# Kernel tuning notes

Hardware: AMD Instinct MI355X
Metric: run time of the kernel (lower is better)

Reference implementation:

```python
import jax, jax.numpy as jnp
import numpy as np


def setup_inputs() -> dict:
    key = jax.random.key(0)
    k1, k2, k3, k4, k5 = jax.random.split(key, 5)
    B, D, T = 32, 256, 32       # batch, word_feature_dim, seq_len
    Dh, H, Wd = 128, 128, 128   # image_feature_dim, height, width
    word_features = jax.random.normal(k1, (B, D, T), dtype=jnp.float32)
    image_features = jax.random.normal(k2, (B, Dh, H, Wd), dtype=jnp.float32)
    words_mask = jax.random.randint(k3, (B, T), 0, 2, dtype=jnp.int32)
    W = jax.random.normal(k4, (Dh, D), dtype=jnp.float32) * (1.0 / np.sqrt(D))
    b = jax.random.normal(k5, (Dh,), dtype=jnp.float32) * 0.01
    return {"word_features": word_features, "image_features": image_features,
            "words_mask": words_mask, "W": W, "b": b}


def reference(word_features, image_features, words_mask, W, b):
    B, D, T = word_features.shape
    Dh = image_features.shape[1]
    N = image_features.shape[2] * image_features.shape[3]  # H*W
    # values = fc(word_features^T)^T : [B, Dh, T]
    values = jnp.einsum('bdt,kd->bkt', word_features, W) + b[None, :, None]
    # queries: [B, N, Dh] (flatten spatial)
    queries = image_features.reshape(B, Dh, N)
    # scores S: [B, N, T]
    S = jnp.einsum('bkn,bkt->bnt', queries, values)
    mask = (words_mask != 0)[:, None, :]  # [B,1,T], True => masked
    S = jnp.where(mask, -jnp.inf, S)
    # softmax over seq dim (original: exp / sum(exp)); stable form is same math
    attn_coefficients = jax.nn.softmax(S, axis=2)  # [B, N, T]
    # context vectors: [B, Dh, N]
    attn = jnp.einsum('bkt,bnt->bkn', values, attn_coefficients)
    return attn, attn_coefficients
```

## Files before the change

### kernel.cpp

```cpp
#include <hip/hip_runtime.h>
#include <math.h>

constexpr int Bc  = 32;
constexpr int Dc  = 256;
constexpr int Tc  = 32;
constexpr int DHc = 128;
constexpr int Nc  = 16384;

typedef _Float16 v8hf __attribute__((ext_vector_type(8)));
typedef _Float16 v2hf __attribute__((ext_vector_type(2)));
typedef float    v4f  __attribute__((ext_vector_type(4)));

__global__ __launch_bounds__(256) void values_kernel(
    const float* __restrict__ wf, const float* __restrict__ Wm,
    const float* __restrict__ bias,
    _Float16* __restrict__ vth, _Float16* __restrict__ vtl,
    _Float16* __restrict__ vph)
{
    __shared__ float wfs[Dc * Tc];
    __shared__ float Ws[16 * 260];

    const int tid = threadIdx.x;
    const int b   = blockIdx.x >> 3;
    const int k0  = (blockIdx.x & 7) * 16;

    {
        const float4* src = (const float4*)(wf + (size_t)b * Dc * Tc);
        float4* dst = (float4*)wfs;
        #pragma unroll
        for (int i = 0; i < 8; ++i) dst[tid + 256 * i] = src[tid + 256 * i];
    }
    {
        #pragma unroll
        for (int i = 0; i < 4; ++i) {
            int f = tid + 256 * i;
            int row = f >> 6, d4 = f & 63;
            *(float4*)&Ws[row * 260 + 4 * d4] =
                *(const float4*)&Wm[(size_t)(k0 + row) * Dc + 4 * d4];
        }
    }
    __syncthreads();

    const int kl  = tid >> 4;
    const int tt0 = (tid & 15) * 2;
    const int k   = k0 + kl;

    float acc0 = bias[k], acc1 = acc0;
    #pragma unroll
    for (int d4 = 0; d4 < 64; ++d4) {
        const float4 w4 = *(const float4*)&Ws[kl * 260 + 4 * d4];
        #pragma unroll
        for (int j = 0; j < 4; ++j) {
            const float2 f2 = *(const float2*)&wfs[(4 * d4 + j) * Tc + tt0];
            const float wv = (j == 0) ? w4.x : (j == 1) ? w4.y : (j == 2) ? w4.z : w4.w;
            acc0 = fmaf(wv, f2.x, acc0);
            acc1 = fmaf(wv, f2.y, acc1);
        }
    }

    _Float16 vh0 = (_Float16)acc0, vh1 = (_Float16)acc1;
    _Float16 vl0 = (_Float16)(acc0 - (float)vh0);
    _Float16 vl1 = (_Float16)(acc1 - (float)vh1);

    __syncthreads();
    _Float16* sh_h = (_Float16*)wfs;
    _Float16* th_h = sh_h + 16 * 32;
    _Float16* th_l = th_h + 32 * 24;

    sh_h[kl * 32 + tt0]     = vh0;
    sh_h[kl * 32 + tt0 + 1] = vh1;
    th_h[tt0 * 24 + kl]       = vh0;
    th_h[(tt0 + 1) * 24 + kl] = vh1;
    th_l[tt0 * 24 + kl]       = vl0;
    th_l[(tt0 + 1) * 24 + kl] = vl1;
    __syncthreads();

    if (tid < 64) {
        int row = tid >> 2, ch = (tid & 3) * 8;
        *(uint4*)&vph[((size_t)b * DHc + k0 + row) * Tc + ch] =
            *(uint4*)&sh_h[row * 32 + ch];
    } else if (tid < 128) {
        int i = tid - 64; int t = i >> 1, hf = (i & 1) * 8;
        *(uint4*)&vth[((size_t)b * Tc + t) * DHc + k0 + hf] =
            *(uint4*)&th_h[t * 24 + hf];
    } else if (tid < 192) {
        int i = tid - 128; int t = i >> 1, hf = (i & 1) * 8;
        *(uint4*)&vtl[((size_t)b * Tc + t) * DHc + k0 + hf] =
            *(uint4*)&th_l[t * 24 + hf];
    }
}

__device__ __forceinline__ _Float16 pick_half(int u, int sel) {
    unsigned short s = (unsigned short)(sel ? (u >> 16) : u);
    return __builtin_bit_cast(_Float16, s);
}

__global__ __launch_bounds__(256) void attn_kernel(
    const float* __restrict__ img,
    const _Float16* __restrict__ vth, const _Float16* __restrict__ vtl,
    const _Float16* __restrict__ vph,
    const int* __restrict__ mask, float* __restrict__ attn,
    float* __restrict__ coeff)
{
    constexpr int VT_LD = 136;
    constexpr int VP_LD = 40;
    __shared__ __align__(16) _Float16 VTh[Tc * VT_LD];
    __shared__ __align__(16) _Float16 VTl[Tc * VT_LD];
    __shared__ __align__(16) _Float16 VPh[DHc * VP_LD];
    __shared__ float mneg[Tc];

    const int tid   = threadIdx.x;
    const int b     = blockIdx.x >> 6;
    const int strip = blockIdx.x & 63;

    {
        const uint4* sth = (const uint4*)(vth + (size_t)b * Tc * DHc);
        const uint4* stl = (const uint4*)(vtl + (size_t)b * Tc * DHc);
        const uint4* sph = (const uint4*)(vph + (size_t)b * DHc * Tc);
        #pragma unroll
        for (int i = 0; i < 2; ++i) {
            int cid = tid + 256 * i;
            int t = cid >> 4, cc = cid & 15;
            *(uint4*)&VTh[t * VT_LD + 8 * cc] = sth[cid];
            *(uint4*)&VTl[t * VT_LD + 8 * cc] = stl[cid];
            int kk = cid >> 2, c4 = cid & 3;
            *(uint4*)&VPh[kk * VP_LD + 8 * c4] = sph[cid];
        }
        if (tid < Tc) mneg[tid] = mask[b * Tc + tid] ? -INFINITY : 0.0f;
    }
    __syncthreads();

    const int lane = tid & 63;
    const int wave = tid >> 6;
    const int c    = lane & 15;
    const int g    = lane >> 4;

    float madd[2][4];
    #pragma unroll
    for (int tt = 0; tt < 2; ++tt)
        #pragma unroll
        for (int r = 0; r < 4; ++r)
            madd[tt][r] = mneg[16 * tt + 4 * g + r];

    const float* qbase = img  + ((size_t)b * DHc + 8 * g) * Nc + c;
    float*       abase = attn + ((size_t)b * DHc + c) * Nc + 4 * g;
    float*       cbase = coeff + (size_t)b * Nc * Tc;

    const int ls_lo = c + 32 * (g & 1);
    const int sel   = g >> 1;

    #pragma unroll 2
    for (int it = 0; it < 4; ++it) {
        const int n0 = strip * 256 + (it * 4 + wave) * 16;

        const float* qp = qbase + n0;
        v8hf Qh[4], Ql[4];
        #pragma unroll
        for (int ks = 0; ks < 4; ++ks)
            #pragma unroll
            for (int j = 0; j < 8; ++j) {
                float qv = qp[(size_t)(ks * 32 + j) * Nc];
                _Float16 h = (_Float16)qv;
                Qh[ks][j] = h;
                Ql[ks][j] = (_Float16)(qv - (float)h);
            }

        v4f Sh[2], Sl[2];
        #pragma unroll
        for (int tt = 0; tt < 2; ++tt) {
            Sh[tt] = (v4f){0.f, 0.f, 0.f, 0.f};
            Sl[tt] = (v4f){0.f, 0.f, 0.f, 0.f};
        }
        #pragma unroll
        for (int tt = 0; tt < 2; ++tt) {
            const int rowbase = (16 * tt + c) * VT_LD + 8 * g;
            #pragma unroll
            for (int ks = 0; ks < 4; ++ks) {
                v8hf va = *(const v8hf*)&VTh[rowbase + ks * 32];
                v8hf vl = *(const v8hf*)&VTl[rowbase + ks * 32];
                Sh[tt] = __builtin_amdgcn_mfma_f32_16x16x32_f16(va, Qh[ks], Sh[tt], 0, 0, 0);
                Sl[tt] = __builtin_amdgcn_mfma_f32_16x16x32_f16(va, Ql[ks], Sl[tt], 0, 0, 0);
                Sl[tt] = __builtin_amdgcn_mfma_f32_16x16x32_f16(vl, Qh[ks], Sl[tt], 0, 0, 0);
            }
        }

        float p0[4], p1[4];
        float m = -INFINITY;
        #pragma unroll
        for (int r = 0; r < 4; ++r) {
            p0[r] = Sh[0][r] + Sl[0][r] + madd[0][r];
            p1[r] = Sh[1][r] + Sl[1][r] + madd[1][r];
            m = fmaxf(m, fmaxf(p0[r], p1[r]));
        }
        m = fmaxf(m, __shfl_xor(m, 16));
        m = fmaxf(m, __shfl_xor(m, 32));
        float sum = 0.0f;
        #pragma unroll
        for (int r = 0; r < 4; ++r) {
            p0[r] = __expf(p0[r] - m); sum += p0[r];
            p1[r] = __expf(p1[r] - m); sum += p1[r];
        }
        sum += __shfl_xor(sum, 16);
        sum += __shfl_xor(sum, 32);
        const float inv = 1.0f / sum;
        #pragma unroll
        for (int r = 0; r < 4; ++r) { p0[r] *= inv; p1[r] *= inv; }

        float* cp = cbase + (size_t)(n0 + c) * Tc + 4 * g;
        *(float4*)cp        = make_float4(p0[0], p0[1], p0[2], p0[3]);
        *(float4*)(cp + 16) = make_float4(p1[0], p1[1], p1[2], p1[3]);

        v8hf Pb;
        #pragma unroll
        for (int r = 0; r < 4; ++r) {
            v2hf h2; h2[0] = (_Float16)p0[r]; h2[1] = (_Float16)p1[r];
            int u   = __builtin_bit_cast(int, h2);
            int ulo = __shfl(u, ls_lo);
            int uhi = __shfl(u, ls_lo + 16);
            Pb[r]     = pick_half(ulo, sel);
            Pb[4 + r] = pick_half(uhi, sel);
        }

        #pragma unroll
        for (int mt = 0; mt < 8; ++mt) {
            v8hf vb2 = *(const v8hf*)&VPh[(16 * mt + c) * VP_LD + 8 * g];
            v4f o = (v4f){0.f, 0.f, 0.f, 0.f};
            o = __builtin_amdgcn_mfma_f32_16x16x32_f16(Pb, vb2, o, 0, 0, 0);
            float* ap = abase + (size_t)(16 * mt) * Nc + n0;
            *(float4*)ap = make_float4(o[0], o[1], o[2], o[3]);
        }
    }
}

extern "C" void kernel_launch(void* const* d_in, const int* in_sizes, int n_in,
                              void* d_out, int out_size, void* d_ws, size_t ws_size,
                              hipStream_t stream)
{
    const float* wf   = (const float*)d_in[0];
    const float* img  = (const float*)d_in[1];
    const int*   msk  = (const int*)d_in[2];
    const float* Wm   = (const float*)d_in[3];
    const float* bias = (const float*)d_in[4];

    float* attn  = (float*)d_out;
    float* coeff = attn + (size_t)Bc * DHc * Nc;

    _Float16* vth = (_Float16*)d_ws;
    _Float16* vtl = vth + (size_t)Bc * DHc * Tc;
    _Float16* vph = vtl + (size_t)Bc * DHc * Tc;

    values_kernel<<<256, 256, 0, stream>>>(wf, Wm, bias, vth, vtl, vph);
    attn_kernel<<<Bc * 64, 256, 0, stream>>>(img, vth, vtl, vph, msk, attn, coeff);
}
```

Baseline: 534.6 us.

## Switch attention kernel to 32x32x16 MFMA tiles with 32-position waves

Reworks the attention kernel so each wave handles 32 spatial positions using 32x32x16 f16 MFMA instructions instead of 16x16x32, for both the score and the context matmuls. The P-matrix relayout now needs one xor-32 shuffle per pair instead of two indexed shuffles with a half-select, and the softmax reductions drop one cross-lane step. All Q loads are hoisted into a register array before conversion. The aim is fewer MFMA issues and shuffles per position and wider 128-byte row segments per global load, at the cost of higher register pressure from the 16-wide accumulators and the 64-float Q buffer.

New measurement: 524.1 us. Within noise of the previous version (-2.0%).

```diff
diff --git a/kernel.cpp b/kernel.cpp
--- a/kernel.cpp
+++ b/kernel.cpp
@@ -10,6 +10,7 @@
 typedef _Float16 v8hf __attribute__((ext_vector_type(8)));
 typedef _Float16 v2hf __attribute__((ext_vector_type(2)));
 typedef float    v4f  __attribute__((ext_vector_type(4)));
+typedef float    v16f __attribute__((ext_vector_type(16)));
 
 __global__ __launch_bounds__(256) void values_kernel(
     const float* __restrict__ wf, const float* __restrict__ Wm,
@@ -88,11 +89,6 @@
         *(uint4*)&vtl[((size_t)b * Tc + t) * DHc + k0 + hf] =
             *(uint4*)&th_l[t * 24 + hf];
     }
-}
-
-__device__ __forceinline__ _Float16 pick_half(int u, int sel) {
-    unsigned short s = (unsigned short)(sel ? (u >> 16) : u);
-    return __builtin_bit_cast(_Float16, s);
 }
 
 __global__ __launch_bounds__(256) void attn_kernel(
@@ -132,102 +128,108 @@
 
     const int lane = tid & 63;
     const int wave = tid >> 6;
-    const int c    = lane & 15;
-    const int g    = lane >> 4;
-
-    float madd[2][4];
+    const int l31  = lane & 31;
+    const int h    = lane >> 5;
+
+    float madd[16];
     #pragma unroll
-    for (int tt = 0; tt < 2; ++tt)
-        #pragma unroll
-        for (int r = 0; r < 4; ++r)
-            madd[tt][r] = mneg[16 * tt + 4 * g + r];
-
-    const float* qbase = img  + ((size_t)b * DHc + 8 * g) * Nc + c;
-    float*       abase = attn + ((size_t)b * DHc + c) * Nc + 4 * g;
+    for (int r = 0; r < 16; ++r)
+        madd[r] = mneg[(r & 3) + 8 * (r >> 2) + 4 * h];
+
+    const float* qbase = img  + ((size_t)b * DHc + 8 * h) * Nc + l31;
     float*       cbase = coeff + (size_t)b * Nc * Tc;
 
-    const int ls_lo = c + 32 * (g & 1);
-    const int sel   = g >> 1;
-
-    #pragma unroll 2
-    for (int it = 0; it < 4; ++it) {
-        const int n0 = strip * 256 + (it * 4 + wave) * 16;
+    for (int it = 0; it < 2; ++it) {
+        const int n0 = strip * 256 + it * 128 + wave * 32;
 
         const float* qp = qbase + n0;
-        v8hf Qh[4], Ql[4];
-        #pragma unroll
-        for (int ks = 0; ks < 4; ++ks)
+        float q[8][8];
+        #pragma unroll
+        for (int ks = 0; ks < 8; ++ks)
+            #pragma unroll
+            for (int j = 0; j < 8; ++j)
+                q[ks][j] = qp[(size_t)(ks * 16 + j) * Nc];
+
+        v8hf Qh[8], Ql[8];
+        #pragma unroll
+        for (int ks = 0; ks < 8; ++ks)
             #pragma unroll
             for (int j = 0; j < 8; ++j) {
-                float qv = qp[(size_t)(ks * 32 + j) * Nc];
-                _Float16 h = (_Float16)qv;
-                Qh[ks][j] = h;
-                Ql[ks][j] = (_Float16)(qv - (float)h);
+                _Float16 hh = (_Float16)q[ks][j];
+                Qh[ks][j] = hh;
+                Ql[ks][j] = (_Float16)(q[ks][j] - (float)hh);
             }
 
-        v4f Sh[2], Sl[2];
-        #pragma unroll
-        for (int tt = 0; tt < 2; ++tt) {
-            Sh[tt] = (v4f){0.f, 0.f, 0.f, 0.f};
-            Sl[tt] = (v4f){0.f, 0.f, 0.f, 0.f};
-        }
-        #pragma unroll
-        for (int tt = 0; tt < 2; ++tt) {
-            const int rowbase = (16 * tt + c) * VT_LD + 8 * g;
-            #pragma unroll
-            for (int ks = 0; ks < 4; ++ks) {
-                v8hf va = *(const v8hf*)&VTh[rowbase + ks * 32];
-                v8hf vl = *(const v8hf*)&VTl[rowbase + ks * 32];
-                Sh[tt] = __builtin_amdgcn_mfma_f32_16x16x32_f16(va, Qh[ks], Sh[tt], 0, 0, 0);
-                Sl[tt] = __builtin_amdgcn_mfma_f32_16x16x32_f16(va, Ql[ks], Sl[tt], 0, 0, 0);
-                Sl[tt] = __builtin_amdgcn_mfma_f32_16x16x32_f16(vl, Qh[ks], Sl[tt], 0, 0, 0);
-            }
-        }
-
-        float p0[4], p1[4];
+        v16f Sh = {0.f}, Sl = {0.f};
+        #pragma unroll
+        for (int r = 0; r < 16; ++r) { Sh[r] = 0.f; Sl[r] = 0.f; }
+        #pragma unroll
+        for (int ks = 0; ks < 8; ++ks) {
+            v8hf va = *(const v8hf*)&VTh[l31 * VT_LD + ks * 16 + 8 * h];
+            v8hf vl = *(const v8hf*)&VTl[l31 * VT_LD + ks * 16 + 8 * h];
+            Sh = __builtin_amdgcn_mfma_f32_32x32x16_f16(va, Qh[ks], Sh, 0, 0, 0);
+            Sl = __builtin_amdgcn_mfma_f32_32x32x16_f16(va, Ql[ks], Sl, 0, 0, 0);
+            Sl = __builtin_amdgcn_mfma_f32_32x32x16_f16(vl, Qh[ks], Sl, 0, 0, 0);
+        }
+
+        float p[16];
         float m = -INFINITY;
         #pragma unroll
-        for (int r = 0; r < 4; ++r) {
-            p0[r] = Sh[0][r] + Sl[0][r] + madd[0][r];
-            p1[r] = Sh[1][r] + Sl[1][r] + madd[1][r];
-            m = fmaxf(m, fmaxf(p0[r], p1[r]));
-        }
-        m = fmaxf(m, __shfl_xor(m, 16));
+        for (int r = 0; r < 16; ++r) {
+            p[r] = Sh[r] + Sl[r] + madd[r];
+            m = fmaxf(m, p[r]);
+        }
         m = fmaxf(m, __shfl_xor(m, 32));
         float sum = 0.0f;
         #pragma unroll
-        for (int r = 0; r < 4; ++r) {
-            p0[r] = __expf(p0[r] - m); sum += p0[r];
-            p1[r] = __expf(p1[r] - m); sum += p1[r];
-        }
-        sum += __shfl_xor(sum, 16);
+        for (int r = 0; r < 16; ++r) {
+            p[r] = __expf(p[r] - m);
+            sum += p[r];
+        }
         sum += __shfl_xor(sum, 32);
         const float inv = 1.0f / sum;
         #pragma unroll
-        for (int r = 0; r < 4; ++r) { p0[r] *= inv; p1[r] *= inv; }
-
-        float* cp = cbase + (size_t)(n0 + c) * Tc + 4 * g;
-        *(float4*)cp        = make_float4(p0[0], p0[1], p0[2], p0[3]);
-        *(float4*)(cp + 16) = make_float4(p1[0], p1[1], p1[2], p1[3]);
-
-        v8hf Pb;
-        #pragma unroll
-        for (int r = 0; r < 4; ++r) {
-            v2hf h2; h2[0] = (_Float16)p0[r]; h2[1] = (_Float16)p1[r];
-            int u   = __builtin_bit_cast(int, h2);
-            int ulo = __shfl(u, ls_lo);
-            int uhi = __shfl(u, ls_lo + 16);
-            Pb[r]     = pick_half(ulo, sel);
-            Pb[4 + r] = pick_half(uhi, sel);
-        }
-
-        #pragma unroll
-        for (int mt = 0; mt < 8; ++mt) {
-            v8hf vb2 = *(const v8hf*)&VPh[(16 * mt + c) * VP_LD + 8 * g];
-            v4f o = (v4f){0.f, 0.f, 0.f, 0.f};
-            o = __builtin_amdgcn_mfma_f32_16x16x32_f16(Pb, vb2, o, 0, 0, 0);
-            float* ap = abase + (size_t)(16 * mt) * Nc + n0;
-            *(float4*)ap = make_float4(o[0], o[1], o[2], o[3]);
+        for (int r = 0; r < 16; ++r) p[r] *= inv;
+
+        {
+            float* cp = cbase + (size_t)(n0 + l31) * Tc + 4 * h;
+            #pragma unroll
+            for (int rg = 0; rg < 4; ++rg)
+                *(float4*)(cp + 8 * rg) =
+                    make_float4(p[4*rg], p[4*rg+1], p[4*rg+2], p[4*rg+3]);
+        }
+
+        int u[8];
+        #pragma unroll
+        for (int i = 0; i < 8; ++i) {
+            v2hf d; d[0] = (_Float16)p[2*i]; d[1] = (_Float16)p[2*i+1];
+            u[i] = __builtin_bit_cast(int, d);
+        }
+        int pu[8];
+        #pragma unroll
+        for (int i = 0; i < 8; ++i) pu[i] = __shfl_xor(u[i], 32);
+
+        int4 a0 = h == 0 ? make_int4(u[0], u[1], pu[0], pu[1])
+                         : make_int4(pu[2], pu[3], u[2], u[3]);
+        int4 a1 = h == 0 ? make_int4(u[4], u[5], pu[4], pu[5])
+                         : make_int4(pu[6], pu[7], u[6], u[7]);
+        v8hf PA0 = __builtin_bit_cast(v8hf, a0);
+        v8hf PA1 = __builtin_bit_cast(v8hf, a1);
+
+        #pragma unroll
+        for (int mt = 0; mt < 4; ++mt) {
+            v8hf vb0 = *(const v8hf*)&VPh[(mt * 32 + l31) * VP_LD + 8 * h];
+            v8hf vb1 = *(const v8hf*)&VPh[(mt * 32 + l31) * VP_LD + 16 + 8 * h];
+            v16f O;
+            #pragma unroll
+            for (int r = 0; r < 16; ++r) O[r] = 0.f;
+            O = __builtin_amdgcn_mfma_f32_32x32x16_f16(PA0, vb0, O, 0, 0, 0);
+            O = __builtin_amdgcn_mfma_f32_32x32x16_f16(PA1, vb1, O, 0, 0, 0);
+            float* ap = attn + ((size_t)b * DHc + mt * 32 + l31) * Nc + n0 + 4 * h;
+            #pragma unroll
+            for (int rg = 0; rg < 4; ++rg)
+                *(float4*)(ap + 8 * rg) =
+                    make_float4(O[4*rg], O[4*rg+1], O[4*rg+2], O[4*rg+3]);
         }
     }
 }
```
